# Kernel optimization log

Hardware: AMD Instinct MI355X
Metric: run time of the kernel (lower is better)

## Reference

```python
import jax, jax.numpy as jnp
import numpy as np

EMBED = 1024
HEADS = 16
HEAD_DIM = EMBED // HEADS
OUT_DIM = 1024


def setup_inputs() -> dict:
    key = jax.random.key(0)
    ks = jax.random.split(key, 8)
    N, L = 2, 2048
    values = jax.random.normal(ks[0], (N, L, EMBED), dtype=jnp.float32)
    keys_t = jax.random.normal(ks[1], (N, L, EMBED), dtype=jnp.float32)
    query = jax.random.normal(ks[2], (N, L, EMBED), dtype=jnp.float32)
    s = 1.0 / np.sqrt(HEAD_DIM)
    Wv = jax.random.normal(ks[3], (HEAD_DIM, HEAD_DIM), dtype=jnp.float32) * s
    Wk = jax.random.normal(ks[4], (HEAD_DIM, HEAD_DIM), dtype=jnp.float32) * s
    Wq = jax.random.normal(ks[5], (HEAD_DIM, HEAD_DIM), dtype=jnp.float32) * s
    Wout = jax.random.normal(ks[6], (OUT_DIM, EMBED), dtype=jnp.float32) * (1.0 / np.sqrt(EMBED))
    bout = jax.random.normal(ks[7], (OUT_DIM,), dtype=jnp.float32) * 0.01
    return {"values": values, "keys": keys_t, "query": query,
            "Wv": Wv, "Wk": Wk, "Wq": Wq, "Wout": Wout, "bout": bout}


def reference(values, keys, query, Wv, Wk, Wq, Wout, bout):
    N, Lq, _ = query.shape
    Lk = keys.shape[1]
    # split into heads: (N, L, H, D)
    v = values.reshape(N, Lk, HEADS, HEAD_DIM)
    k = keys.reshape(N, Lk, HEADS, HEAD_DIM)
    q = query.reshape(N, Lq, HEADS, HEAD_DIM)
    # per-head shared linear projections (torch Linear: x @ W.T, no bias)
    v = jnp.einsum('nlhd,ed->nlhe', v, Wv)
    k = jnp.einsum('nlhd,ed->nlhe', k, Wk)
    q = jnp.einsum('nqhd,ed->nqhe', q, Wq)
    # scores (N, H, Q, K); NOTE: scale is 1/sqrt(embed_size), per original code
    scores = jnp.einsum('nqhd,nkhd->nhqk', q, k) / jnp.sqrt(jnp.float32(EMBED))
    attn = jax.nn.softmax(scores, axis=-1)
    out = jnp.einsum('nhqk,nkhd->nqhd', attn, v).reshape(N, Lq, EMBED)
    # fc_out: x @ Wout.T + bout
    return out @ Wout.T + bout
```

## Files before the change

kernel.cpp:

```cpp
#include <hip/hip_runtime.h>
#include <cstdint>

typedef __attribute__((ext_vector_type(8))) short short8;
typedef __attribute__((ext_vector_type(4))) float floatx4;

#define DEV __device__ __forceinline__

constexpr int NB = 2, Lseq = 2048, NH = 16, HD = 64, EMB = 1024;
constexpr float QSCALE = 0.03125f * 1.4426950408889634f;

DEV uint16_t f2bf(float f) {
  uint32_t x = __builtin_bit_cast(uint32_t, f);
  x += 0x7fffu + ((x >> 16) & 1u);
  return (uint16_t)(x >> 16);
}

DEV uint32_t pack2(float lo, float hi) {
  uint32_t a = __builtin_bit_cast(uint32_t, lo) + 0x8000u;
  uint32_t b = __builtin_bit_cast(uint32_t, hi) + 0x8000u;
  return __builtin_amdgcn_perm(b, a, 0x07060302);
}

DEV void gl_lds16(const void* g, void* l) {
  __builtin_amdgcn_global_load_lds((const __attribute__((address_space(1))) void*)g,
                                   (__attribute__((address_space(3))) void*)l, 16, 0, 0);
}

DEV short8 ld8bf(const float* p, float sc) {
  float4 u = *(const float4*)p;
  float4 v = *(const float4*)(p + 4);
  union { short8 s; uint32_t d[4]; } r;
  r.d[0] = pack2(u.x * sc, u.y * sc);
  r.d[1] = pack2(u.z * sc, u.w * sc);
  r.d[2] = pack2(v.x * sc, v.y * sc);
  r.d[3] = pack2(v.z * sc, v.w * sc);
  return r.s;
}

__global__ __launch_bounds__(256) void prep_kernel(
    const float* __restrict__ values, const float* __restrict__ keysrc,
    const float* __restrict__ query, const float* __restrict__ Wv,
    const float* __restrict__ Wk, const float* __restrict__ Wq,
    const float* __restrict__ Wout,
    uint16_t* __restrict__ qp, uint16_t* __restrict__ kp,
    uint16_t* __restrict__ vp, uint16_t* __restrict__ wbf) {
  const int t = threadIdx.x, w = t >> 6, lane = t & 63;
  const int quad = lane >> 4, l16 = lane & 15;
  const int wid = blockIdx.x * 4 + w;
  const int mat = wid >> 10, sub = wid & 1023;

  if (mat == 3) {
#pragma unroll
    for (int i = 0; i < 4; ++i) {
      int idx = sub * 256 + i * 64 + lane;
      float4 v = ((const float4*)Wout)[idx];
      uint2 p;
      p.x = pack2(v.x, v.y);
      p.y = pack2(v.z, v.w);
      ((uint2*)wbf)[idx] = p;
    }
    return;
  }

  floatx4 c[4][4];
#pragma unroll
  for (int i = 0; i < 4; ++i)
#pragma unroll
    for (int j = 0; j < 4; ++j) c[i][j] = floatx4{0.f, 0.f, 0.f, 0.f};

  if (mat < 2) {
    const float* src = mat ? keysrc : query;
    const float* W   = mat ? Wk : Wq;
    const float bsc  = mat ? 1.f : QSCALE;
    uint16_t* dst    = mat ? kp : qp;
    const int R0 = sub * 64;
    short8 a[4][2], b[4][2];
#pragma unroll
    for (int dc = 0; dc < 2; ++dc) {
#pragma unroll
      for (int f = 0; f < 4; ++f) {
        a[f][dc] = ld8bf(src + (size_t)(R0 + f * 16 + l16) * 64 + dc * 32 + quad * 8, 1.f);
        b[f][dc] = ld8bf(W + (size_t)(f * 16 + l16) * 64 + dc * 32 + quad * 8, bsc);
      }
    }
#pragma unroll
    for (int dc = 0; dc < 2; ++dc)
#pragma unroll
      for (int mf = 0; mf < 4; ++mf)
#pragma unroll
        for (int nf = 0; nf < 4; ++nf)
          c[mf][nf] = __builtin_amdgcn_mfma_f32_16x16x32_bf16(a[mf][dc], b[nf][dc], c[mf][nf], 0, 0, 0);
#pragma unroll
    for (int mf = 0; mf < 4; ++mf) {
#pragma unroll
      for (int rr = 0; rr < 4; ++rr) {
        int r = R0 + mf * 16 + quad * 4 + rr;
        int h = r & 15, l = (r >> 4) & 2047, n = r >> 15;
        uint16_t* drow = dst + ((size_t)(n * 16 + h) * 2048 + l) * 64;
#pragma unroll
        for (int nf = 0; nf < 4; ++nf) drow[nf * 16 + l16] = f2bf(c[mf][nf][rr]);
      }
    }
  } else {
    const int nh = sub >> 5, L0 = (sub & 31) * 64;
    const int n = nh >> 4, h = nh & 15;
    short8 a[4][2], b[4][2];
#pragma unroll
    for (int dc = 0; dc < 2; ++dc) {
#pragma unroll
      for (int f = 0; f < 4; ++f) {
        a[f][dc] = ld8bf(Wv + (size_t)(f * 16 + l16) * 64 + dc * 32 + quad * 8, 1.f);
        b[f][dc] = ld8bf(values + (size_t)(n * 2048 + L0 + f * 16 + l16) * 1024 + h * 64 + dc * 32 + quad * 8, 1.f);
      }
    }
#pragma unroll
    for (int dc = 0; dc < 2; ++dc)
#pragma unroll
      for (int mf = 0; mf < 4; ++mf)
#pragma unroll
        for (int nf = 0; nf < 4; ++nf)
          c[mf][nf] = __builtin_amdgcn_mfma_f32_16x16x32_bf16(a[mf][dc], b[nf][dc], c[mf][nf], 0, 0, 0);
#pragma unroll
    for (int mf = 0; mf < 4; ++mf) {
#pragma unroll
      for (int rr = 0; rr < 4; ++rr) {
        int d = mf * 16 + quad * 4 + rr;
        uint16_t* drow = vp + ((size_t)nh * 64 + d) * 2048 + L0;
#pragma unroll
        for (int nf = 0; nf < 4; ++nf) drow[nf * 16 + l16] = f2bf(c[mf][nf][rr]);
      }
    }
  }
}

__global__ __launch_bounds__(256) void flash_kernel(const uint16_t* __restrict__ qp,
                                                    const uint16_t* __restrict__ kp,
                                                    const uint16_t* __restrict__ vp,
                                                    uint16_t* __restrict__ xatt,
                                                    float* __restrict__ opart,
                                                    float* __restrict__ psum_g,
                                                    int kbn) {
  __shared__ uint16_t Kt[2][64 * 64];
  __shared__ uint16_t Vt[2][64 * 64];
  __shared__ uint16_t Pt[4][32 * 72];
  const int t = threadIdx.x;
  const int w = t >> 6, lane = t & 63, quad = lane >> 4, l16 = lane & 15;
  const int nh = blockIdx.y, qt = blockIdx.x, kh = blockIdx.z;
  const int q0 = qt * 128 + w * 32;
  const uint16_t* Qb = qp + (size_t)nh * Lseq * HD;
  const uint16_t* Kb = kp + (size_t)nh * Lseq * HD + (size_t)kh * kbn * 64 * 64;
  const uint16_t* Vb = vp + (size_t)nh * HD * Lseq;
  const int vcol0 = kh * kbn * 64;
  const int srow = lane >> 3, sc8 = (lane & 7) ^ (lane >> 3);

  short8 bq[2][2];
#pragma unroll
  for (int qb = 0; qb < 2; ++qb) {
    bq[qb][0] = *(const short8*)(Qb + (q0 + qb * 16 + l16) * 64 + quad * 8);
    bq[qb][1] = *(const short8*)(Qb + (q0 + qb * 16 + l16) * 64 + 32 + quad * 8);
  }

  floatx4 o[4][2];
  float psum[2] = {0.f, 0.f};
#pragma unroll
  for (int i = 0; i < 4; ++i)
#pragma unroll
    for (int qb = 0; qb < 2; ++qb) o[i][qb] = floatx4{0.f, 0.f, 0.f, 0.f};

#pragma unroll
  for (int i = 0; i < 2; ++i) {
    int r0 = w * 16 + i * 8;
    gl_lds16(Kb + (r0 + srow) * 64 + sc8 * 8, &Kt[0][r0 * 64]);
    gl_lds16(Vb + (size_t)(r0 + srow) * Lseq + vcol0 + sc8 * 8, &Vt[0][r0 * 64]);
  }

  for (int kb = 0; kb < kbn; ++kb) {
    __syncthreads();
    const int cur = kb & 1;
    if (kb + 1 < kbn) {
      const int nxt = cur ^ 1;
      const uint16_t* kg = Kb + (kb + 1) * (64 * 64);
#pragma unroll
      for (int i = 0; i < 2; ++i) {
        int r0 = w * 16 + i * 8;
        gl_lds16(kg + (r0 + srow) * 64 + sc8 * 8, &Kt[nxt][r0 * 64]);
        gl_lds16(Vb + (size_t)(r0 + srow) * Lseq + vcol0 + (kb + 1) * 64 + sc8 * 8, &Vt[nxt][r0 * 64]);
      }
    }

    floatx4 s[4][2];
#pragma unroll
    for (int kb16 = 0; kb16 < 4; ++kb16)
#pragma unroll
      for (int qb = 0; qb < 2; ++qb) s[kb16][qb] = floatx4{0.f, 0.f, 0.f, 0.f};
#pragma unroll
    for (int dc = 0; dc < 2; ++dc) {
#pragma unroll
      for (int kb16 = 0; kb16 < 4; ++kb16) {
        int row = kb16 * 16 + l16;
        short8 ak = *(const short8*)(&Kt[cur][row * 64 + ((dc * 4 + quad) ^ (row & 7)) * 8]);
        s[kb16][0] = __builtin_amdgcn_mfma_f32_16x16x32_bf16(ak, bq[0][dc], s[kb16][0], 0, 0, 0);
        s[kb16][1] = __builtin_amdgcn_mfma_f32_16x16x32_bf16(ak, bq[1][dc], s[kb16][1], 0, 0, 0);
      }
    }

#pragma unroll
    for (int qb = 0; qb < 2; ++qb) {
      uint16_t* pw = &Pt[w][(qb * 16 + l16) * 72];
#pragma unroll
      for (int kb16 = 0; kb16 < 4; ++kb16) {
        float p0 = __builtin_amdgcn_exp2f(s[kb16][qb][0]);
        float p1 = __builtin_amdgcn_exp2f(s[kb16][qb][1]);
        float p2 = __builtin_amdgcn_exp2f(s[kb16][qb][2]);
        float p3 = __builtin_amdgcn_exp2f(s[kb16][qb][3]);
        psum[qb] += (p0 + p1) + (p2 + p3);
        uint2 pk;
        pk.x = pack2(p0, p1);
        pk.y = pack2(p2, p3);
        *(uint2*)(pw + kb16 * 16 + quad * 4) = pk;
      }
    }

    short8 bp[2][2];
#pragma unroll
    for (int qb = 0; qb < 2; ++qb)
#pragma unroll
      for (int kc = 0; kc < 2; ++kc)
        bp[qb][kc] = *(const short8*)(&Pt[w][(qb * 16 + l16) * 72 + kc * 32 + quad * 8]);
#pragma unroll
    for (int kc = 0; kc < 2; ++kc) {
#pragma unroll
      for (int db = 0; db < 4; ++db) {
        int row = db * 16 + l16;
        short8 av = *(const short8*)(&Vt[cur][row * 64 + ((kc * 4 + quad) ^ (row & 7)) * 8]);
        o[db][0] = __builtin_amdgcn_mfma_f32_16x16x32_bf16(av, bp[0][kc], o[db][0], 0, 0, 0);
        o[db][1] = __builtin_amdgcn_mfma_f32_16x16x32_bf16(av, bp[1][kc], o[db][1], 0, 0, 0);
      }
    }
  }

  if (opart) {
    float* ob = opart + (((size_t)nh * 16 + qt) * 2 + kh) * 8192 + (size_t)w * 8 * 256;
#pragma unroll
    for (int db = 0; db < 4; ++db)
#pragma unroll
      for (int qb = 0; qb < 2; ++qb)
        *(floatx4*)(ob + (db * 2 + qb) * 256 + lane * 4) = o[db][qb];
#pragma unroll
    for (int qb = 0; qb < 2; ++qb) {
      float l = psum[qb];
      l += __shfl_xor(l, 16, 64);
      l += __shfl_xor(l, 32, 64);
      if (quad == 0)
        psum_g[(((size_t)nh * 16 + qt) * 2 + kh) * 128 + w * 32 + qb * 16 + l16] = l;
    }
  } else {
    const int n = nh >> 4, h = nh & 15;
#pragma unroll
    for (int qb = 0; qb < 2; ++qb) {
      float l = psum[qb];
      l += __shfl_xor(l, 16, 64);
      l += __shfl_xor(l, 32, 64);
      float inv = 1.f / l;
      size_t rowb = (size_t)(n * Lseq + q0 + qb * 16 + l16) * EMB + h * 64;
#pragma unroll
      for (int db = 0; db < 4; ++db) {
        uint2 pk;
        pk.x = pack2(o[db][qb][0] * inv, o[db][qb][1] * inv);
        pk.y = pack2(o[db][qb][2] * inv, o[db][qb][3] * inv);
        *(uint2*)(xatt + rowb + db * 16 + quad * 4) = pk;
      }
    }
  }
}

__global__ __launch_bounds__(256) void combine_kernel(const float* __restrict__ opart,
                                                      const float* __restrict__ psum_g,
                                                      uint16_t* __restrict__ xatt) {
  const int t = threadIdx.x, w = t >> 6, lane = t & 63, quad = lane >> 4, l16 = lane & 15;
  const int qt = blockIdx.x, nh = blockIdx.y;
  const int n = nh >> 4, h = nh & 15;
  const size_t tb = ((size_t)nh * 16 + qt) * 2;
  const float* oa = opart + tb * 8192 + (size_t)w * 8 * 256;
  const float* ob = opart + (tb + 1) * 8192 + (size_t)w * 8 * 256;
  float inv[2];
#pragma unroll
  for (int qb = 0; qb < 2; ++qb) {
    int q = w * 32 + qb * 16 + l16;
    inv[qb] = 1.f / (psum_g[tb * 128 + q] + psum_g[(tb + 1) * 128 + q]);
  }
#pragma unroll
  for (int db = 0; db < 4; ++db)
#pragma unroll
    for (int qb = 0; qb < 2; ++qb) {
      floatx4 a = *(const floatx4*)(oa + (db * 2 + qb) * 256 + lane * 4);
      floatx4 b = *(const floatx4*)(ob + (db * 2 + qb) * 256 + lane * 4);
      float v0 = (a[0] + b[0]) * inv[qb];
      float v1 = (a[1] + b[1]) * inv[qb];
      float v2 = (a[2] + b[2]) * inv[qb];
      float v3 = (a[3] + b[3]) * inv[qb];
      uint2 pk;
      pk.x = pack2(v0, v1);
      pk.y = pack2(v2, v3);
      size_t row = (size_t)(n * Lseq + qt * 128 + w * 32 + qb * 16 + l16) * EMB + h * 64;
      *(uint2*)(xatt + row + db * 16 + quad * 4) = pk;
    }
}

__global__ __launch_bounds__(256) void gemm_out_kernel(const uint16_t* __restrict__ X,
                                                       const uint16_t* __restrict__ Wb,
                                                       const float* __restrict__ bias,
                                                       float* __restrict__ out) {
  __shared__ uint16_t Xt[2][128 * 64];
  __shared__ uint16_t Wt[2][64 * 64];
  const int t = threadIdx.x, w = t >> 6, lane = t & 63, quad = lane >> 4, l16 = lane & 15;
  const int m0 = blockIdx.y * 128, o0 = blockIdx.x * 64;
  const int srow = lane >> 3, sc8 = (lane & 7) ^ (lane >> 3);
  floatx4 c[2][4];
#pragma unroll
  for (int i = 0; i < 2; ++i)
#pragma unroll
    for (int j = 0; j < 4; ++j) c[i][j] = floatx4{0.f, 0.f, 0.f, 0.f};

#pragma unroll
  for (int i = 0; i < 4; ++i) {
    int r0 = w * 32 + i * 8;
    gl_lds16(X + (size_t)(m0 + r0 + srow) * 1024 + sc8 * 8, &Xt[0][r0 * 64]);
  }
#pragma unroll
  for (int i = 0; i < 2; ++i) {
    int r0 = w * 16 + i * 8;
    gl_lds16(Wb + (size_t)(o0 + r0 + srow) * 1024 + sc8 * 8, &Wt[0][r0 * 64]);
  }

  for (int kt = 0; kt < 16; ++kt) {
    __syncthreads();
    const int cur = kt & 1;
    if (kt + 1 < 16) {
      const int nxt = cur ^ 1;
      const int e0 = (kt + 1) * 64;
#pragma unroll
      for (int i = 0; i < 4; ++i) {
        int r0 = w * 32 + i * 8;
        gl_lds16(X + (size_t)(m0 + r0 + srow) * 1024 + e0 + sc8 * 8, &Xt[nxt][r0 * 64]);
      }
#pragma unroll
      for (int i = 0; i < 2; ++i) {
        int r0 = w * 16 + i * 8;
        gl_lds16(Wb + (size_t)(o0 + r0 + srow) * 1024 + e0 + sc8 * 8, &Wt[nxt][r0 * 64]);
      }
    }
#pragma unroll
    for (int kc = 0; kc < 2; ++kc) {
      short8 a[2], b[4];
#pragma unroll
      for (int mf = 0; mf < 2; ++mf) {
        int row = w * 32 + mf * 16 + l16;
        a[mf] = *(const short8*)(&Xt[cur][row * 64 + ((kc * 4 + quad) ^ (row & 7)) * 8]);
      }
#pragma unroll
      for (int nf = 0; nf < 4; ++nf) {
        int rw = nf * 16 + l16;
        b[nf] = *(const short8*)(&Wt[cur][rw * 64 + ((kc * 4 + quad) ^ (rw & 7)) * 8]);
      }
#pragma unroll
      for (int mf = 0; mf < 2; ++mf)
#pragma unroll
        for (int nf = 0; nf < 4; ++nf)
          c[mf][nf] = __builtin_amdgcn_mfma_f32_16x16x32_bf16(a[mf], b[nf], c[mf][nf], 0, 0, 0);
    }
  }
#pragma unroll
  for (int nf = 0; nf < 4; ++nf) {
    float bv = bias[o0 + nf * 16 + l16];
#pragma unroll
    for (int mf = 0; mf < 2; ++mf)
#pragma unroll
      for (int r = 0; r < 4; ++r)
        out[(size_t)(m0 + w * 32 + mf * 16 + quad * 4 + r) * 1024 + o0 + nf * 16 + l16] =
            c[mf][nf][r] + bv;
  }
}

extern "C" void kernel_launch(void* const* d_in, const int* in_sizes, int n_in,
                              void* d_out, int out_size, void* d_ws, size_t ws_size,
                              hipStream_t stream) {
  const float* values = (const float*)d_in[0];
  const float* keys   = (const float*)d_in[1];
  const float* query  = (const float*)d_in[2];
  const float* Wv     = (const float*)d_in[3];
  const float* Wk     = (const float*)d_in[4];
  const float* Wq     = (const float*)d_in[5];
  const float* Wout   = (const float*)d_in[6];
  const float* bout   = (const float*)d_in[7];
  float* out = (float*)d_out;

  uint16_t* ws  = (uint16_t*)d_ws;
  uint16_t* qp  = ws;
  uint16_t* kp  = ws + (size_t)4194304;
  uint16_t* vp  = ws + (size_t)2 * 4194304;
  uint16_t* xat = ws + (size_t)3 * 4194304;
  uint16_t* wbf = ws + (size_t)4 * 4194304;
  float* opart  = (float*)(ws + (size_t)17825792);
  float* psum   = opart + (size_t)8388608;
  const bool split = ws_size >= 69730304ull;

  prep_kernel<<<dim3(1024), dim3(256), 0, stream>>>(values, keys, query, Wv, Wk, Wq, Wout,
                                                    qp, kp, vp, wbf);
  if (split) {
    flash_kernel<<<dim3(16, 32, 2), dim3(256), 0, stream>>>(qp, kp, vp, nullptr, opart, psum, 16);
    combine_kernel<<<dim3(16, 32), dim3(256), 0, stream>>>(opart, psum, xat);
  } else {
    flash_kernel<<<dim3(16, 32, 1), dim3(256), 0, stream>>>(qp, kp, vp, xat, nullptr, nullptr, 32);
  }
  gemm_out_kernel<<<dim3(16, 32), dim3(256), 0, stream>>>(xat, wbf, bout, out);
}
```

Measured before the change: 188.0 us.

## Read K/V tiles directly from global memory instead of double-buffered LDS

Removes the LDS double-buffered K and V staging and the per-iteration block barrier, so each wave loads its MFMA operands for K and V straight from global memory, relying on L1/L2 reuse across the four waves. Adds a launch-bounds occupancy hint of three blocks per CU, which the lower LDS footprint makes possible. The tradeoff is that each wave now fetches K/V redundantly and without the latency hiding of the prefetch, exchanged for no synchronisation and higher occupancy.

```diff
diff --git a/kernel.cpp b/kernel.cpp
--- a/kernel.cpp
+++ b/kernel.cpp
@@ -133,15 +133,13 @@
   }
 }
 
-__global__ __launch_bounds__(256) void flash_kernel(const uint16_t* __restrict__ qp,
-                                                    const uint16_t* __restrict__ kp,
-                                                    const uint16_t* __restrict__ vp,
-                                                    uint16_t* __restrict__ xatt,
-                                                    float* __restrict__ opart,
-                                                    float* __restrict__ psum_g,
-                                                    int kbn) {
-  __shared__ uint16_t Kt[2][64 * 64];
-  __shared__ uint16_t Vt[2][64 * 64];
+__global__ __launch_bounds__(256, 3) void flash_kernel(const uint16_t* __restrict__ qp,
+                                                       const uint16_t* __restrict__ kp,
+                                                       const uint16_t* __restrict__ vp,
+                                                       uint16_t* __restrict__ xatt,
+                                                       float* __restrict__ opart,
+                                                       float* __restrict__ psum_g,
+                                                       int kbn) {
   __shared__ uint16_t Pt[4][32 * 72];
   const int t = threadIdx.x;
   const int w = t >> 6, lane = t & 63, quad = lane >> 4, l16 = lane & 15;
@@ -149,9 +147,7 @@
   const int q0 = qt * 128 + w * 32;
   const uint16_t* Qb = qp + (size_t)nh * Lseq * HD;
   const uint16_t* Kb = kp + (size_t)nh * Lseq * HD + (size_t)kh * kbn * 64 * 64;
-  const uint16_t* Vb = vp + (size_t)nh * HD * Lseq;
-  const int vcol0 = kh * kbn * 64;
-  const int srow = lane >> 3, sc8 = (lane & 7) ^ (lane >> 3);
+  const uint16_t* Vb = vp + (size_t)nh * HD * Lseq + (size_t)kh * kbn * 64;
 
   short8 bq[2][2];
 #pragma unroll
@@ -167,26 +163,9 @@
 #pragma unroll
     for (int qb = 0; qb < 2; ++qb) o[i][qb] = floatx4{0.f, 0.f, 0.f, 0.f};
 
-#pragma unroll
-  for (int i = 0; i < 2; ++i) {
-    int r0 = w * 16 + i * 8;
-    gl_lds16(Kb + (r0 + srow) * 64 + sc8 * 8, &Kt[0][r0 * 64]);
-    gl_lds16(Vb + (size_t)(r0 + srow) * Lseq + vcol0 + sc8 * 8, &Vt[0][r0 * 64]);
-  }
-
   for (int kb = 0; kb < kbn; ++kb) {
-    __syncthreads();
-    const int cur = kb & 1;
-    if (kb + 1 < kbn) {
-      const int nxt = cur ^ 1;
-      const uint16_t* kg = Kb + (kb + 1) * (64 * 64);
-#pragma unroll
-      for (int i = 0; i < 2; ++i) {
-        int r0 = w * 16 + i * 8;
-        gl_lds16(kg + (r0 + srow) * 64 + sc8 * 8, &Kt[nxt][r0 * 64]);
-        gl_lds16(Vb + (size_t)(r0 + srow) * Lseq + vcol0 + (kb + 1) * 64 + sc8 * 8, &Vt[nxt][r0 * 64]);
-      }
-    }
+    const uint16_t* kt = Kb + (size_t)kb * (64 * 64);
+    const uint16_t* vt = Vb + (size_t)kb * 64;
 
     floatx4 s[4][2];
 #pragma unroll
@@ -197,8 +176,7 @@
     for (int dc = 0; dc < 2; ++dc) {
 #pragma unroll
       for (int kb16 = 0; kb16 < 4; ++kb16) {
-        int row = kb16 * 16 + l16;
-        short8 ak = *(const short8*)(&Kt[cur][row * 64 + ((dc * 4 + quad) ^ (row & 7)) * 8]);
+        short8 ak = *(const short8*)(kt + (kb16 * 16 + l16) * 64 + dc * 32 + quad * 8);
         s[kb16][0] = __builtin_amdgcn_mfma_f32_16x16x32_bf16(ak, bq[0][dc], s[kb16][0], 0, 0, 0);
         s[kb16][1] = __builtin_amdgcn_mfma_f32_16x16x32_bf16(ak, bq[1][dc], s[kb16][1], 0, 0, 0);
       }
@@ -227,12 +205,12 @@
 #pragma unroll
       for (int kc = 0; kc < 2; ++kc)
         bp[qb][kc] = *(const short8*)(&Pt[w][(qb * 16 + l16) * 72 + kc * 32 + quad * 8]);
+
 #pragma unroll
     for (int kc = 0; kc < 2; ++kc) {
 #pragma unroll
       for (int db = 0; db < 4; ++db) {
-        int row = db * 16 + l16;
-        short8 av = *(const short8*)(&Vt[cur][row * 64 + ((kc * 4 + quad) ^ (row & 7)) * 8]);
+        short8 av = *(const short8*)(vt + (size_t)(db * 16 + l16) * Lseq + kc * 32 + quad * 8);
         o[db][0] = __builtin_amdgcn_mfma_f32_16x16x32_bf16(av, bp[0][kc], o[db][0], 0, 0, 0);
         o[db][1] = __builtin_amdgcn_mfma_f32_16x16x32_bf16(av, bp[1][kc], o[db][1], 0, 0, 0);
       }
```

After: 254.8 us. 35.5% more time.

## Keep softmax probabilities in registers via fp16 16x16x16 MFMA for PV

Applied to the files above, without the earlier changes.

The attention kernel no longer stages P through per-wave LDS. Exponentiated scores are packed to fp16 in registers and fed straight into 16x16x16 f16 MFMAs, whose accumulator layout lines up with the operand layout, so the LDS write/read round trip goes away. V is now stored as fp16 to match. The projection kernel swaps MFMA operand roles so it can write packed 8-byte vector stores instead of scalar ones. Launch bounds ask for 3 blocks per CU; the cost is twice as many, smaller MFMAs for PV, plus fp16 range and precision limits on P and V.

```diff
diff --git a/kernel.cpp b/kernel.cpp
--- a/kernel.cpp
+++ b/kernel.cpp
@@ -3,6 +3,8 @@
 
 typedef __attribute__((ext_vector_type(8))) short short8;
 typedef __attribute__((ext_vector_type(4))) float floatx4;
+typedef __attribute__((ext_vector_type(4))) _Float16 half4;
+typedef __attribute__((ext_vector_type(2))) __fp16 fp16x2;
 
 #define DEV __device__ __forceinline__
 
@@ -19,6 +21,10 @@
   uint32_t a = __builtin_bit_cast(uint32_t, lo) + 0x8000u;
   uint32_t b = __builtin_bit_cast(uint32_t, hi) + 0x8000u;
   return __builtin_amdgcn_perm(b, a, 0x07060302);
+}
+
+DEV uint32_t packh2(float lo, float hi) {
+  return __builtin_bit_cast(uint32_t, __builtin_amdgcn_cvt_pkrtz(lo, hi));
 }
 
 DEV void gl_lds16(const void* g, void* l) {
@@ -71,7 +77,7 @@
   if (mat < 2) {
     const float* src = mat ? keysrc : query;
     const float* W   = mat ? Wk : Wq;
-    const float bsc  = mat ? 1.f : QSCALE;
+    const float asc  = mat ? 1.f : QSCALE;
     uint16_t* dst    = mat ? kp : qp;
     const int R0 = sub * 64;
     short8 a[4][2], b[4][2];
@@ -79,8 +85,8 @@
     for (int dc = 0; dc < 2; ++dc) {
 #pragma unroll
       for (int f = 0; f < 4; ++f) {
-        a[f][dc] = ld8bf(src + (size_t)(R0 + f * 16 + l16) * 64 + dc * 32 + quad * 8, 1.f);
-        b[f][dc] = ld8bf(W + (size_t)(f * 16 + l16) * 64 + dc * 32 + quad * 8, bsc);
+        a[f][dc] = ld8bf(W + (size_t)(f * 16 + l16) * 64 + dc * 32 + quad * 8, asc);
+        b[f][dc] = ld8bf(src + (size_t)(R0 + f * 16 + l16) * 64 + dc * 32 + quad * 8, 1.f);
       }
     }
 #pragma unroll
@@ -91,14 +97,16 @@
         for (int nf = 0; nf < 4; ++nf)
           c[mf][nf] = __builtin_amdgcn_mfma_f32_16x16x32_bf16(a[mf][dc], b[nf][dc], c[mf][nf], 0, 0, 0);
 #pragma unroll
-    for (int mf = 0; mf < 4; ++mf) {
-#pragma unroll
-      for (int rr = 0; rr < 4; ++rr) {
-        int r = R0 + mf * 16 + quad * 4 + rr;
-        int h = r & 15, l = (r >> 4) & 2047, n = r >> 15;
-        uint16_t* drow = dst + ((size_t)(n * 16 + h) * 2048 + l) * 64;
-#pragma unroll
-        for (int nf = 0; nf < 4; ++nf) drow[nf * 16 + l16] = f2bf(c[mf][nf][rr]);
+    for (int nf = 0; nf < 4; ++nf) {
+      int r = R0 + nf * 16 + l16;
+      int h = r & 15, l = (r >> 4) & 2047, n = r >> 15;
+      uint16_t* drow = dst + ((size_t)(n * 16 + h) * 2048 + l) * 64;
+#pragma unroll
+      for (int mf = 0; mf < 4; ++mf) {
+        uint2 pk;
+        pk.x = pack2(c[mf][nf][0], c[mf][nf][1]);
+        pk.y = pack2(c[mf][nf][2], c[mf][nf][3]);
+        *(uint2*)(drow + mf * 16 + quad * 4) = pk;
       }
     }
   } else {
@@ -109,8 +117,8 @@
     for (int dc = 0; dc < 2; ++dc) {
 #pragma unroll
       for (int f = 0; f < 4; ++f) {
-        a[f][dc] = ld8bf(Wv + (size_t)(f * 16 + l16) * 64 + dc * 32 + quad * 8, 1.f);
-        b[f][dc] = ld8bf(values + (size_t)(n * 2048 + L0 + f * 16 + l16) * 1024 + h * 64 + dc * 32 + quad * 8, 1.f);
+        a[f][dc] = ld8bf(values + (size_t)(n * 2048 + L0 + f * 16 + l16) * 1024 + h * 64 + dc * 32 + quad * 8, 1.f);
+        b[f][dc] = ld8bf(Wv + (size_t)(f * 16 + l16) * 64 + dc * 32 + quad * 8, 1.f);
       }
     }
 #pragma unroll
@@ -121,28 +129,29 @@
         for (int nf = 0; nf < 4; ++nf)
           c[mf][nf] = __builtin_amdgcn_mfma_f32_16x16x32_bf16(a[mf][dc], b[nf][dc], c[mf][nf], 0, 0, 0);
 #pragma unroll
-    for (int mf = 0; mf < 4; ++mf) {
-#pragma unroll
-      for (int rr = 0; rr < 4; ++rr) {
-        int d = mf * 16 + quad * 4 + rr;
-        uint16_t* drow = vp + ((size_t)nh * 64 + d) * 2048 + L0;
-#pragma unroll
-        for (int nf = 0; nf < 4; ++nf) drow[nf * 16 + l16] = f2bf(c[mf][nf][rr]);
-      }
-    }
-  }
-}
-
-__global__ __launch_bounds__(256) void flash_kernel(const uint16_t* __restrict__ qp,
-                                                    const uint16_t* __restrict__ kp,
-                                                    const uint16_t* __restrict__ vp,
-                                                    uint16_t* __restrict__ xatt,
-                                                    float* __restrict__ opart,
-                                                    float* __restrict__ psum_g,
-                                                    int kbn) {
+    for (int nf = 0; nf < 4; ++nf) {
+      int d = nf * 16 + l16;
+      uint16_t* drow = vp + ((size_t)nh * 64 + d) * 2048 + L0;
+#pragma unroll
+      for (int mf = 0; mf < 4; ++mf) {
+        uint2 pk;
+        pk.x = packh2(c[mf][nf][0], c[mf][nf][1]);
+        pk.y = packh2(c[mf][nf][2], c[mf][nf][3]);
+        *(uint2*)(drow + mf * 16 + quad * 4) = pk;
+      }
+    }
+  }
+}
+
+__global__ __launch_bounds__(256, 3) void flash_kernel(const uint16_t* __restrict__ qp,
+                                                       const uint16_t* __restrict__ kp,
+                                                       const uint16_t* __restrict__ vp,
+                                                       uint16_t* __restrict__ xatt,
+                                                       float* __restrict__ opart,
+                                                       float* __restrict__ psum_g,
+                                                       int kbn) {
   __shared__ uint16_t Kt[2][64 * 64];
   __shared__ uint16_t Vt[2][64 * 64];
-  __shared__ uint16_t Pt[4][32 * 72];
   const int t = threadIdx.x;
   const int w = t >> 6, lane = t & 63, quad = lane >> 4, l16 = lane & 15;
   const int nh = blockIdx.y, qt = blockIdx.x, kh = blockIdx.z;
@@ -204,9 +213,9 @@
       }
     }
 
+    half4 bp[4][2];
 #pragma unroll
     for (int qb = 0; qb < 2; ++qb) {
-      uint16_t* pw = &Pt[w][(qb * 16 + l16) * 72];
 #pragma unroll
       for (int kb16 = 0; kb16 < 4; ++kb16) {
         float p0 = __builtin_amdgcn_exp2f(s[kb16][qb][0]);
@@ -214,27 +223,22 @@
         float p2 = __builtin_amdgcn_exp2f(s[kb16][qb][2]);
         float p3 = __builtin_amdgcn_exp2f(s[kb16][qb][3]);
         psum[qb] += (p0 + p1) + (p2 + p3);
-        uint2 pk;
-        pk.x = pack2(p0, p1);
-        pk.y = pack2(p2, p3);
-        *(uint2*)(pw + kb16 * 16 + quad * 4) = pk;
-      }
-    }
-
-    short8 bp[2][2];
-#pragma unroll
-    for (int qb = 0; qb < 2; ++qb)
-#pragma unroll
-      for (int kc = 0; kc < 2; ++kc)
-        bp[qb][kc] = *(const short8*)(&Pt[w][(qb * 16 + l16) * 72 + kc * 32 + quad * 8]);
-#pragma unroll
-    for (int kc = 0; kc < 2; ++kc) {
+        union { half4 h4; uint32_t d[2]; } u;
+        u.d[0] = packh2(p0, p1);
+        u.d[1] = packh2(p2, p3);
+        bp[kb16][qb] = u.h4;
+      }
+    }
+
+#pragma unroll
+    for (int kb16 = 0; kb16 < 4; ++kb16) {
 #pragma unroll
       for (int db = 0; db < 4; ++db) {
         int row = db * 16 + l16;
-        short8 av = *(const short8*)(&Vt[cur][row * 64 + ((kc * 4 + quad) ^ (row & 7)) * 8]);
-        o[db][0] = __builtin_amdgcn_mfma_f32_16x16x32_bf16(av, bp[0][kc], o[db][0], 0, 0, 0);
-        o[db][1] = __builtin_amdgcn_mfma_f32_16x16x32_bf16(av, bp[1][kc], o[db][1], 0, 0, 0);
+        int ch = (kb16 * 2 + (quad >> 1)) ^ (row & 7);
+        half4 av = *(const half4*)(&Vt[cur][row * 64 + ch * 8 + (quad & 1) * 4]);
+        o[db][0] = __builtin_amdgcn_mfma_f32_16x16x16f16(av, bp[kb16][0], o[db][0], 0, 0, 0);
+        o[db][1] = __builtin_amdgcn_mfma_f32_16x16x16f16(av, bp[kb16][1], o[db][1], 0, 0, 0);
       }
     }
   }
```

Result: faster. 183.2 us (-2.6%).
